# Performance work log

Hardware: AMD Instinct MI355X
Metric: run time of the kernel (lower is better)

## Reference

```python
import jax, jax.numpy as jnp
import numpy as np

N = 100000
IN_C = 128
OUT_C = 32
HEADS = 4
E = 1600000
NEG_SLOPE = 0.2


def setup_inputs() -> dict:
    key = jax.random.key(0)
    ks = jax.random.split(key, 8)
    x = jax.random.normal(ks[0], (N, IN_C), dtype=jnp.float32)
    edge_index = jax.random.randint(ks[1], (2, E), 0, N, dtype=jnp.int64)
    # GATConv params (PyG conventions): lin weight [H*C, in], att vectors [H, C], bias [H*C]
    sc = 1.0 / np.sqrt(IN_C)
    W = jax.random.uniform(ks[2], (HEADS * OUT_C, IN_C), dtype=jnp.float32, minval=-sc, maxval=sc)
    att_src = jax.random.normal(ks[3], (HEADS, OUT_C), dtype=jnp.float32) * 0.1
    att_dst = jax.random.normal(ks[4], (HEADS, OUT_C), dtype=jnp.float32) * 0.1
    bias_conv = jnp.zeros((HEADS * OUT_C,), dtype=jnp.float32)
    # final nn.Linear(H*C, C)
    sl = 1.0 / np.sqrt(HEADS * OUT_C)
    W_lin = jax.random.uniform(ks[5], (OUT_C, HEADS * OUT_C), dtype=jnp.float32, minval=-sl, maxval=sl)
    b_lin = jax.random.uniform(ks[6], (OUT_C,), dtype=jnp.float32, minval=-sl, maxval=sl)
    return {"x": x, "edge_index": edge_index, "W": W, "att_src": att_src,
            "att_dst": att_dst, "bias_conv": bias_conv, "W_lin": W_lin, "b_lin": b_lin}


def reference(x, edge_index, W, att_src, att_dst, bias_conv, W_lin, b_lin):
    n = x.shape[0]
    # add self loops (PyG default)
    loops = jnp.arange(n, dtype=edge_index.dtype)
    src = jnp.concatenate([edge_index[0], loops])
    dst = jnp.concatenate([edge_index[1], loops])
    # linear projection, per-head split: [N, H, C]
    h = (x @ W.T).reshape(n, HEADS, OUT_C)
    # per-node attention logits
    a_src = jnp.einsum('nhc,hc->nh', h, att_src)  # [N, H]
    a_dst = jnp.einsum('nhc,hc->nh', h, att_dst)  # [N, H]
    e = a_src[src] + a_dst[dst]                   # [E', H]
    e = jax.nn.leaky_relu(e, NEG_SLOPE)
    # segment softmax over incoming edges per destination node
    m = jax.ops.segment_max(e, dst, num_segments=n)       # [N, H]
    e = jnp.exp(e - m[dst])
    s = jax.ops.segment_sum(e, dst, num_segments=n)       # [N, H]
    alpha = e / s[dst]                                    # [E', H]
    # scatter-aggregate alpha-weighted source features
    msg = alpha[:, :, None] * h[src]                      # [E', H, C]
    out = jax.ops.segment_sum(msg, dst, num_segments=n)   # [N, H, C]
    out = out.reshape(n, HEADS * OUT_C) + bias_conv
    # final linear + ELU
    return jax.nn.elu(out @ W_lin.T + b_lin)
```

## Files before the change

### kernel.cpp

```cpp
#include <hip/hip_runtime.h>
#include <hip/hip_fp16.h>
#include <cstdint>
#include <cstddef>

#define NHEADS 4
#define OUT_C 32
#define HC 128
#define IN_CH 128
#define NEG_SLOPE 0.2f
#define LDSPAD 136
#define KEDGE 4096

typedef _Float16 half8 __attribute__((ext_vector_type(8)));
typedef float floatx4 __attribute__((ext_vector_type(4)));

static inline size_t align256(size_t v) { return (v + 255) & ~(size_t)255; }

__device__ __forceinline__ float lrelu(float v) { return v > 0.f ? v : NEG_SLOPE * v; }

__device__ __forceinline__ float wred_sum(float v) {
    v += __shfl_xor(v, 1);
    v += __shfl_xor(v, 2);
    v += __shfl_xor(v, 4);
    v += __shfl_xor(v, 8);
    v += __shfl_xor(v, 16);
    v += __shfl_xor(v, 32);
    return v;
}

__device__ __forceinline__ unsigned int pack_h2(float a, float b) {
    __half2 h = __floats2half2_rn(a, b);
    return *reinterpret_cast<unsigned int*>(&h);
}
__device__ __forceinline__ float2 unpack_h2(unsigned int u) {
    __half2 h = *reinterpret_cast<__half2*>(&u);
    return __half22float2(h);
}

__global__ void dw(const float* __restrict__ W, _Float16* __restrict__ wh,
                   const int* __restrict__ ei, int* __restrict__ flag) {
    if (blockIdx.x < 64) {
        int idx = blockIdx.x * 256 + threadIdx.x;
        wh[idx] = (_Float16)W[idx];
        return;
    }
    __shared__ int red[256];
    int t = threadIdx.x;
    int acc = 0;
    for (int i = t; i < 1024; i += 256) acc |= ei[2 * i + 1];
    red[t] = acc;
    __syncthreads();
    for (int s = 128; s > 0; s >>= 1) {
        if (t < s) red[t] |= red[t + s];
        __syncthreads();
    }
    if (t == 0) *flag = (red[0] == 0) ? 1 : 0;
}

__global__ __launch_bounds__(256) void gemm_h(const float* __restrict__ x,
                                              const _Float16* __restrict__ wh,
                                              const float* __restrict__ att_src,
                                              const float* __restrict__ att_dst,
                                              __half* __restrict__ h,
                                              float* __restrict__ a_src,
                                              float* __restrict__ a_dst, int n) {
    __shared__ __align__(16) _Float16 Ws[128 * LDSPAD];
    __shared__ __align__(16) _Float16 Xs[128 * LDSPAD];
    int tid = threadIdx.x;
    int rowbase = blockIdx.x << 7;

    const uint4* w4 = (const uint4*)wh;
#pragma unroll
    for (int i = 0; i < 8; ++i) {
        int u = (i << 8) + tid;
        int r = u >> 4, g = u & 15;
        uint4 v = w4[u];
        *(uint4*)&Ws[r * LDSPAD + (g << 3)] = v;
    }
    const float4* x4 = (const float4*)x;
#pragma unroll
    for (int i = 0; i < 16; ++i) {
        int u = (i << 8) + tid;
        int r = u >> 5, c4 = u & 31;
        int row = rowbase + r;
        if (row >= n) row = n - 1;
        float4 v = x4[((size_t)row << 5) + c4];
        uint2 uu;
        uu.x = pack_h2(v.x, v.y);
        uu.y = pack_h2(v.z, v.w);
        *(uint2*)&Xs[r * LDSPAD + (c4 << 2)] = uu;
    }
    __syncthreads();

    int lane = tid & 63, w = tid >> 6;
    int quad = lane >> 4, Lm = lane & 15;
    floatx4 acc[2][8];
#pragma unroll
    for (int rt = 0; rt < 2; ++rt)
#pragma unroll
        for (int c = 0; c < 8; ++c) acc[rt][c] = (floatx4){0.f, 0.f, 0.f, 0.f};

#pragma unroll
    for (int kc = 0; kc < 128; kc += 32) {
        int ko = kc + (quad << 3);
        half8 a0 = *(const half8*)&Xs[((w << 5) + Lm) * LDSPAD + ko];
        half8 a1 = *(const half8*)&Xs[((w << 5) + 16 + Lm) * LDSPAD + ko];
#pragma unroll
        for (int c = 0; c < 8; ++c) {
            half8 b = *(const half8*)&Ws[((c << 4) + Lm) * LDSPAD + ko];
            acc[0][c] = __builtin_amdgcn_mfma_f32_16x16x32_f16(a0, b, acc[0][c], 0, 0, 0);
            acc[1][c] = __builtin_amdgcn_mfma_f32_16x16x32_f16(a1, b, acc[1][c], 0, 0, 0);
        }
    }
    __syncthreads();
#pragma unroll
    for (int rt = 0; rt < 2; ++rt)
#pragma unroll
        for (int c = 0; c < 8; ++c)
#pragma unroll
            for (int i = 0; i < 4; ++i) {
                int rl = (w << 5) + (rt << 4) + (quad << 2) + i;
                int cl = (c << 4) + Lm;
                Xs[rl * LDSPAD + cl] = (_Float16)acc[rt][c][i];
            }
    __syncthreads();
#pragma unroll
    for (int i = 0; i < 8; ++i) {
        int u = (i << 8) + tid;
        int r = u >> 4, g = u & 15;
        int row = rowbase + r;
        if (row < n) {
            uint4 v = *(uint4*)&Xs[r * LDSPAD + (g << 3)];
            *(uint4*)(h + ((size_t)row << 7) + (g << 3)) = v;
        }
    }
    int r = tid >> 1, seg = tid & 1;
    int row = rowbase + r;
    const _Float16* hp = &Xs[r * LDSPAD + (seg << 6)];
    float sa = 0.f, da = 0.f, sb = 0.f, db = 0.f;
#pragma unroll
    for (int g8 = 0; g8 < 8; ++g8) {
        half8 v = *(const half8*)&hp[g8 << 3];
        int co = (seg << 6) + (g8 << 3);
        float4 A1 = *(const float4*)&att_src[co];
        float4 A2 = *(const float4*)&att_src[co + 4];
        float4 D1 = *(const float4*)&att_dst[co];
        float4 D2 = *(const float4*)&att_dst[co + 4];
        float f0 = (float)v[0], f1 = (float)v[1], f2 = (float)v[2], f3 = (float)v[3];
        float f4 = (float)v[4], f5 = (float)v[5], f6 = (float)v[6], f7 = (float)v[7];
        float ts = f0 * A1.x + f1 * A1.y + f2 * A1.z + f3 * A1.w
                 + f4 * A2.x + f5 * A2.y + f6 * A2.z + f7 * A2.w;
        float td = f0 * D1.x + f1 * D1.y + f2 * D1.z + f3 * D1.w
                 + f4 * D2.x + f5 * D2.y + f6 * D2.z + f7 * D2.w;
        if (g8 < 4) { sa += ts; da += td; } else { sb += ts; db += td; }
    }
    if (row < n) {
        int base = (row << 2) + (seg << 1);
        a_src[base] = sa;
        a_src[base + 1] = sb;
        a_dst[base] = da;
        a_dst[base + 1] = db;
    }
}

__global__ void bhist(const int* __restrict__ ei, const int* __restrict__ flag,
                      int* __restrict__ bcount, int E, int sh) {
    __shared__ int c[256];
    int t = threadIdx.x;
    c[t] = 0;
    __syncthreads();
    int f64 = *flag;
    int stride = gridDim.x * 256;
    for (int i = blockIdx.x * 256 + t; i < E; i += stride) {
        int d;
        if (f64) d = (int)((const long long*)ei)[(size_t)E + i];
        else     d = ei[(size_t)E + i];
        atomicAdd(&c[d >> sh], 1);
    }
    __syncthreads();
    if (c[t]) atomicAdd(&bcount[t], c[t]);
}

__global__ void bscan(const int* __restrict__ bcount, int* __restrict__ bucket_base,
                      int* __restrict__ gcursor, int* __restrict__ off,
                      int n, int E, int sh) {
    __shared__ int ts[256];
    int t = threadIdx.x;
    int lo = t << sh, hi = (t + 1) << sh;
    if (hi > n) hi = n;
    int nodes = hi > lo ? hi - lo : 0;
    int v = bcount[t] + nodes;
    ts[t] = v;
    __syncthreads();
    int run = v;
    for (int d = 1; d < 256; d <<= 1) {
        int o = (t >= d) ? ts[t - d] : 0;
        __syncthreads();
        run += o;
        ts[t] = run;
        __syncthreads();
    }
    int excl = run - v;
    bucket_base[t] = excl;
    gcursor[t] = excl;
    if (t == 255) {
        bucket_base[256] = run;
        off[n] = E + n;
    }
}

__global__ __launch_bounds__(256) void bscatter(const int* __restrict__ ei,
                                                const int* __restrict__ flag,
                                                int* __restrict__ gcursor,
                                                int2* __restrict__ bkt,
                                                int E, int n, int sh) {
    __shared__ int cnt[256], base[256], lcur[256];
    int t = threadIdx.x;
    cnt[t] = 0;
    lcur[t] = 0;
    int total = E + n;
    int i0 = blockIdx.x * KEDGE;
    int f64 = *flag;
    int ed[16], es[16];
    __syncthreads();
#pragma unroll
    for (int j = 0; j < 16; ++j) {
        int i = i0 + (j << 8) + t;
        int s = 0, d = -1;
        if (i < total) {
            if (i < E) {
                if (f64) {
                    s = (int)((const long long*)ei)[i];
                    d = (int)((const long long*)ei)[(size_t)E + i];
                } else {
                    s = ei[i];
                    d = ei[(size_t)E + i];
                }
            } else {
                s = d = i - E;
            }
            atomicAdd(&cnt[d >> sh], 1);
        }
        ed[j] = d;
        es[j] = s;
    }
    __syncthreads();
    base[t] = cnt[t] ? atomicAdd(&gcursor[t], cnt[t]) : 0;
    __syncthreads();
#pragma unroll
    for (int j = 0; j < 16; ++j) {
        int d = ed[j];
        if (d >= 0) {
            int b = d >> sh;
            int pos = base[b] + atomicAdd(&lcur[b], 1);
            bkt[pos] = make_int2(d, es[j]);
        }
    }
}

__global__ __launch_bounds__(256) void bsort(const int2* __restrict__ bkt,
                                             const int* __restrict__ bucket_base,
                                             int* __restrict__ off,
                                             int* __restrict__ sorted,
                                             int n, int sh) {
    __shared__ int cnt[512], offl[512], ts[256];
    int t = threadIdx.x, bid = blockIdx.x;
    int node0 = bid << sh;
    int node1 = (bid + 1) << sh;
    if (node1 > n) node1 = n;
    int nn = node1 - node0;
    int e0 = bucket_base[bid], e1 = bucket_base[bid + 1];
    cnt[t] = 0;
    cnt[t + 256] = 0;
    __syncthreads();
    for (int i = e0 + t; i < e1; i += 256) {
        int2 e = bkt[i];
        atomicAdd(&cnt[e.x - node0], 1);
    }
    __syncthreads();
    int a = cnt[t << 1], b = cnt[(t << 1) + 1];
    int s = a + b;
    ts[t] = s;
    __syncthreads();
    int run = s;
    for (int d = 1; d < 256; d <<= 1) {
        int o = (t >= d) ? ts[t - d] : 0;
        __syncthreads();
        run += o;
        ts[t] = run;
        __syncthreads();
    }
    int excl = run - s;
    offl[t << 1] = excl;
    offl[(t << 1) + 1] = excl + a;
    cnt[t << 1] = 0;
    cnt[(t << 1) + 1] = 0;
    __syncthreads();
    for (int i = t; i < nn; i += 256) off[node0 + i] = e0 + offl[i];
    for (int i = e0 + t; i < e1; i += 256) {
        int2 e = bkt[i];
        int li = e.x - node0;
        int pos = e0 + offl[li] + atomicAdd(&cnt[li], 1);
        sorted[pos] = e.y;
    }
}

__device__ __forceinline__ void accum_half(const int* ssrc, const float* sal,
                                           const __half* __restrict__ h,
                                           int deg, int half, int L, int head,
                                           float4& acc) {
    float4 a0 = {0, 0, 0, 0}, a1 = {0, 0, 0, 0}, a2 = {0, 0, 0, 0}, a3 = {0, 0, 0, 0};
    int j = half;
    for (; j + 6 < deg; j += 8) {
        int s0 = ssrc[j], s1 = ssrc[j + 2], s2 = ssrc[j + 4], s3 = ssrc[j + 6];
        float w0 = sal[(j << 2) + head];
        float w1 = sal[((j + 2) << 2) + head];
        float w2 = sal[((j + 4) << 2) + head];
        float w3 = sal[((j + 6) << 2) + head];
        uint2 u0 = *(const uint2*)(h + ((size_t)s0 << 7) + (L << 2));
        uint2 u1 = *(const uint2*)(h + ((size_t)s1 << 7) + (L << 2));
        uint2 u2 = *(const uint2*)(h + ((size_t)s2 << 7) + (L << 2));
        uint2 u3 = *(const uint2*)(h + ((size_t)s3 << 7) + (L << 2));
        float2 f0a = unpack_h2(u0.x), f0b = unpack_h2(u0.y);
        float2 f1a = unpack_h2(u1.x), f1b = unpack_h2(u1.y);
        float2 f2a = unpack_h2(u2.x), f2b = unpack_h2(u2.y);
        float2 f3a = unpack_h2(u3.x), f3b = unpack_h2(u3.y);
        a0.x = fmaf(w0, f0a.x, a0.x); a0.y = fmaf(w0, f0a.y, a0.y);
        a0.z = fmaf(w0, f0b.x, a0.z); a0.w = fmaf(w0, f0b.y, a0.w);
        a1.x = fmaf(w1, f1a.x, a1.x); a1.y = fmaf(w1, f1a.y, a1.y);
        a1.z = fmaf(w1, f1b.x, a1.z); a1.w = fmaf(w1, f1b.y, a1.w);
        a2.x = fmaf(w2, f2a.x, a2.x); a2.y = fmaf(w2, f2a.y, a2.y);
        a2.z = fmaf(w2, f2b.x, a2.z); a2.w = fmaf(w2, f2b.y, a2.w);
        a3.x = fmaf(w3, f3a.x, a3.x); a3.y = fmaf(w3, f3a.y, a3.y);
        a3.z = fmaf(w3, f3b.x, a3.z); a3.w = fmaf(w3, f3b.y, a3.w);
    }
    for (; j < deg; j += 2) {
        int s0 = ssrc[j];
        float w0 = sal[(j << 2) + head];
        uint2 u0 = *(const uint2*)(h + ((size_t)s0 << 7) + (L << 2));
        float2 f0a = unpack_h2(u0.x), f0b = unpack_h2(u0.y);
        a0.x = fmaf(w0, f0a.x, a0.x); a0.y = fmaf(w0, f0a.y, a0.y);
        a0.z = fmaf(w0, f0b.x, a0.z); a0.w = fmaf(w0, f0b.y, a0.w);
    }
    acc.x += a0.x + a1.x + a2.x + a3.x;
    acc.y += a0.y + a1.y + a2.y + a3.y;
    acc.z += a0.z + a1.z + a2.z + a3.z;
    acc.w += a0.w + a1.w + a2.w + a3.w;
}

__global__ __launch_bounds__(256) void aggregate(const __half* __restrict__ h,
                                                 const int* __restrict__ sorted,
                                                 const int* __restrict__ off,
                                                 const float* __restrict__ a_src,
                                                 const float* __restrict__ a_dst,
                                                 const float* __restrict__ bias,
                                                 __half* __restrict__ agg, int n) {
    __shared__ __align__(16) int sh_src[4][64];
    __shared__ __align__(16) float sh_al[4][256];
    int wslot = threadIdx.x >> 6;
    int lane = threadIdx.x & 63;
    int wid = blockIdx.x * 4 + wslot;
    int nw = gridDim.x * 4;
    int L = lane & 31, half = lane >> 5, head = L >> 3;
    float4 b4 = ((const float4*)bias)[L];
    const float4* as4 = (const float4*)a_src;
    const float4* ad4 = (const float4*)a_dst;
    int* ssrc = sh_src[wslot];
    float* sal = sh_al[wslot];

    for (int node = wid; node < n; node += nw) {
        int start = off[node], end = off[node + 1];
        int deg = end - start;
        float4 ad = ad4[node];
        float4 acc = {0.f, 0.f, 0.f, 0.f};
        float4 psum = {0.f, 0.f, 0.f, 0.f};

        if (deg <= 64) {
            bool v = lane < deg;
            int idx = start + (v ? lane : 0);
            int s = sorted[idx];
            float4 as = as4[s];
            float4 p;
            p.x = v ? __expf(lrelu(as.x + ad.x)) : 0.f;
            p.y = v ? __expf(lrelu(as.y + ad.y)) : 0.f;
            p.z = v ? __expf(lrelu(as.z + ad.z)) : 0.f;
            p.w = v ? __expf(lrelu(as.w + ad.w)) : 0.f;
            psum = p;
            ssrc[lane] = s;
            *(float4*)&sal[lane << 2] = p;
            asm volatile("s_waitcnt lgkmcnt(0)" ::: "memory");
            accum_half(ssrc, sal, h, deg, half, L, head, acc);
            asm volatile("" ::: "memory");
        } else {
            for (int bb = 0; bb < deg; bb += 64) {
                int i = bb + lane;
                bool v = i < deg;
                int idx = start + (v ? i : 0);
                int s = sorted[idx];
                float4 as = as4[s];
                float4 p;
                p.x = v ? __expf(lrelu(as.x + ad.x)) : 0.f;
                p.y = v ? __expf(lrelu(as.y + ad.y)) : 0.f;
                p.z = v ? __expf(lrelu(as.z + ad.z)) : 0.f;
                p.w = v ? __expf(lrelu(as.w + ad.w)) : 0.f;
                psum.x += p.x; psum.y += p.y; psum.z += p.z; psum.w += p.w;
                ssrc[lane] = s;
                *(float4*)&sal[lane << 2] = p;
                asm volatile("s_waitcnt lgkmcnt(0)" ::: "memory");
                int cl = deg - bb;
                if (cl > 64) cl = 64;
                accum_half(ssrc, sal, h, cl, half, L, head, acc);
                asm volatile("" ::: "memory");
            }
        }
        float s0 = wred_sum(psum.x), s1 = wred_sum(psum.y);
        float s2 = wred_sum(psum.z), s3 = wred_sum(psum.w);
        float sh = (head == 0) ? s0 : (head == 1) ? s1 : (head == 2) ? s2 : s3;
        float inv = 1.f / sh;
        acc.x += __shfl_xor(acc.x, 32);
        acc.y += __shfl_xor(acc.y, 32);
        acc.z += __shfl_xor(acc.z, 32);
        acc.w += __shfl_xor(acc.w, 32);
        if (lane < 32) {
            float4 res = {fmaf(acc.x, inv, b4.x), fmaf(acc.y, inv, b4.y),
                          fmaf(acc.z, inv, b4.z), fmaf(acc.w, inv, b4.w)};
            uint2 u;
            u.x = pack_h2(res.x, res.y);
            u.y = pack_h2(res.z, res.w);
            *(uint2*)(agg + ((size_t)node << 7) + (L << 2)) = u;
        }
    }
}

__global__ __launch_bounds__(256) void proj(const __half* __restrict__ agg,
                                            const float* __restrict__ W_lin,
                                            const float* __restrict__ b_lin,
                                            float* __restrict__ out, int n) {
    __shared__ float xs[64][132];
    __shared__ float wt[128][36];
    int tid = threadIdx.x;
    const float4* w4 = (const float4*)W_lin;
#pragma unroll
    for (int i = 0; i < 4; ++i) {
        int f4 = (i << 8) + tid;
        int o = f4 >> 5, kk = (f4 & 31) << 2;
        float4 w = w4[f4];
        wt[kk][o] = w.x;
        wt[kk + 1][o] = w.y;
        wt[kk + 2][o] = w.z;
        wt[kk + 3][o] = w.w;
    }
    int rowbase = blockIdx.x << 6;
    const uint4* a4 = (const uint4*)agg;
#pragma unroll
    for (int i = 0; i < 4; ++i) {
        int f8 = (i << 8) + tid;
        int r = f8 >> 4, cc = (f8 & 15) << 3;
        int row = rowbase + r;
        if (row >= n) row = n - 1;
        uint4 u = a4[((size_t)row << 4) + (cc >> 3)];
        float2 f0 = unpack_h2(u.x), f1 = unpack_h2(u.y);
        float2 f2 = unpack_h2(u.z), f3 = unpack_h2(u.w);
        float* xp = &xs[r][cc];
        xp[0] = f0.x; xp[1] = f0.y; xp[2] = f1.x; xp[3] = f1.y;
        xp[4] = f2.x; xp[5] = f2.y; xp[6] = f3.x; xp[7] = f3.y;
    }
    __syncthreads();
    int r = tid >> 2, cg = tid & 3, c0 = cg << 3;
    float acc[8];
#pragma unroll
    for (int j = 0; j < 8; ++j) acc[j] = 0.f;
    for (int k = 0; k < 128; k += 4) {
        float4 xv = *(const float4*)&xs[r][k];
        float xk[4] = {xv.x, xv.y, xv.z, xv.w};
#pragma unroll
        for (int kk = 0; kk < 4; ++kk) {
            float4 wa = *(const float4*)&wt[k + kk][c0];
            float4 wb = *(const float4*)&wt[k + kk][c0 + 4];
            acc[0] = fmaf(xk[kk], wa.x, acc[0]);
            acc[1] = fmaf(xk[kk], wa.y, acc[1]);
            acc[2] = fmaf(xk[kk], wa.z, acc[2]);
            acc[3] = fmaf(xk[kk], wa.w, acc[3]);
            acc[4] = fmaf(xk[kk], wb.x, acc[4]);
            acc[5] = fmaf(xk[kk], wb.y, acc[5]);
            acc[6] = fmaf(xk[kk], wb.z, acc[6]);
            acc[7] = fmaf(xk[kk], wb.w, acc[7]);
        }
    }
    int row = rowbase + r;
    if (row < n) {
        float res[8];
#pragma unroll
        for (int j = 0; j < 8; ++j) {
            float v = acc[j] + b_lin[c0 + j];
            res[j] = v > 0.f ? v : (__expf(v) - 1.f);
        }
        float4* op = (float4*)(out + (size_t)row * 32 + c0);
        op[0] = make_float4(res[0], res[1], res[2], res[3]);
        op[1] = make_float4(res[4], res[5], res[6], res[7]);
    }
}

extern "C" void kernel_launch(void* const* d_in, const int* in_sizes, int n_in,
                              void* d_out, int out_size, void* d_ws, size_t ws_size,
                              hipStream_t stream) {
    const float* x = (const float*)d_in[0];
    const int* ei = (const int*)d_in[1];
    const float* W = (const float*)d_in[2];
    const float* att_src = (const float*)d_in[3];
    const float* att_dst = (const float*)d_in[4];
    const float* bias_conv = (const float*)d_in[5];
    const float* W_lin = (const float*)d_in[6];
    const float* b_lin = (const float*)d_in[7];
    int n = in_sizes[0] / IN_CH;
    int E = in_sizes[1] / 2;

    int sh = 0;
    while (((n + (1 << sh) - 1) >> sh) > 256) sh++;
    int NB = (n + (1 << sh) - 1) >> sh;

    char* ws = (char*)d_ws;
    size_t o = 0;
    auto alloc = [&](size_t bytes) { char* p = ws + o; o = align256(o + bytes); return p; };
    __half* h        = (__half*)alloc((size_t)n * HC * 2);
    __half* agg      = (__half*)alloc((size_t)n * HC * 2);
    _Float16* wh     = (_Float16*)alloc(128 * 128 * 2);
    float* a_src     = (float*)alloc((size_t)n * NHEADS * 4);
    float* a_dst     = (float*)alloc((size_t)n * NHEADS * 4);
    int* off         = (int*)alloc(((size_t)n + 1) * 4);
    int* bcount      = (int*)alloc(256 * 4);
    int* bucket_base = (int*)alloc(257 * 4);
    int* gcursor     = (int*)alloc(256 * 4);
    int* flag        = (int*)alloc(256);
    int* sorted      = (int*)alloc((size_t)(E + n + 64) * 4);
    int2* bkt        = (int2*)alloc((size_t)(E + n + 64) * 8);

    hipMemsetAsync(bcount, 0, 256 * 4, stream);

    dw<<<65, 256, 0, stream>>>(W, wh, ei, flag);
    gemm_h<<<(n + 127) / 128, 256, 0, stream>>>(x, wh, att_src, att_dst, h, a_src, a_dst, n);
    bhist<<<1024, 256, 0, stream>>>(ei, flag, bcount, E, sh);
    bscan<<<1, 256, 0, stream>>>(bcount, bucket_base, gcursor, off, n, E, sh);
    bscatter<<<(E + n + KEDGE - 1) / KEDGE, 256, 0, stream>>>(ei, flag, gcursor, bkt, E, n, sh);
    bsort<<<NB, 256, 0, stream>>>(bkt, bucket_base, off, sorted, n, sh);
    aggregate<<<2048, 256, 0, stream>>>(h, sorted, off, a_src, a_dst, bias_conv, agg, n);
    proj<<<(n + 63) / 64, 256, 0, stream>>>(agg, W_lin, b_lin, (float*)d_out, n);
}
```

Measured before the change: 309.6 us.

## Slice h/agg into per-16-channel planes and fold small kernels into neighbors

```diff
diff --git a/kernel.cpp b/kernel.cpp
--- a/kernel.cpp
+++ b/kernel.cpp
@@ -37,31 +37,29 @@
     return __half22float2(h);
 }
 
-__global__ void dw(const float* __restrict__ W, _Float16* __restrict__ wh,
-                   const int* __restrict__ ei, int* __restrict__ flag) {
-    if (blockIdx.x < 64) {
-        int idx = blockIdx.x * 256 + threadIdx.x;
-        wh[idx] = (_Float16)W[idx];
-        return;
-    }
-    __shared__ int red[256];
+__device__ __forceinline__ int detect_f64(const int* __restrict__ ei, int E, int* sf) {
     int t = threadIdx.x;
+    if (t == 0) *sf = 0;
+    __syncthreads();
+    int lim = E < 1024 ? E : 1024;
     int acc = 0;
-    for (int i = t; i < 1024; i += 256) acc |= ei[2 * i + 1];
-    red[t] = acc;
-    __syncthreads();
-    for (int s = 128; s > 0; s >>= 1) {
-        if (t < s) red[t] |= red[t + s];
-        __syncthreads();
-    }
-    if (t == 0) *flag = (red[0] == 0) ? 1 : 0;
+    for (int i = t; i < lim; i += 256) acc |= ei[2 * i + 1];
+    acc |= __shfl_xor(acc, 1);
+    acc |= __shfl_xor(acc, 2);
+    acc |= __shfl_xor(acc, 4);
+    acc |= __shfl_xor(acc, 8);
+    acc |= __shfl_xor(acc, 16);
+    acc |= __shfl_xor(acc, 32);
+    if ((t & 63) == 0 && acc) atomicOr(sf, 1);
+    __syncthreads();
+    return *sf == 0;
 }
 
 __global__ __launch_bounds__(256) void gemm_h(const float* __restrict__ x,
-                                              const _Float16* __restrict__ wh,
+                                              const float* __restrict__ W,
                                               const float* __restrict__ att_src,
                                               const float* __restrict__ att_dst,
-                                              __half* __restrict__ h,
+                                              __half* __restrict__ hpl,
                                               float* __restrict__ a_src,
                                               float* __restrict__ a_dst, int n) {
     __shared__ __align__(16) _Float16 Ws[128 * LDSPAD];
@@ -69,13 +67,16 @@
     int tid = threadIdx.x;
     int rowbase = blockIdx.x << 7;
 
-    const uint4* w4 = (const uint4*)wh;
-#pragma unroll
-    for (int i = 0; i < 8; ++i) {
+    const float4* wf = (const float4*)W;
+#pragma unroll
+    for (int i = 0; i < 16; ++i) {
         int u = (i << 8) + tid;
-        int r = u >> 4, g = u & 15;
-        uint4 v = w4[u];
-        *(uint4*)&Ws[r * LDSPAD + (g << 3)] = v;
+        int r = u >> 5, g = u & 31;
+        float4 v = wf[u];
+        uint2 uu;
+        uu.x = pack_h2(v.x, v.y);
+        uu.y = pack_h2(v.z, v.w);
+        *(uint2*)&Ws[r * LDSPAD + (g << 2)] = uu;
     }
     const float4* x4 = (const float4*)x;
 #pragma unroll
@@ -124,14 +125,15 @@
                 Xs[rl * LDSPAD + cl] = (_Float16)acc[rt][c][i];
             }
     __syncthreads();
-#pragma unroll
-    for (int i = 0; i < 8; ++i) {
-        int u = (i << 8) + tid;
-        int r = u >> 4, g = u & 15;
+    {
+        int r = tid >> 1, g = tid & 1;
         int row = rowbase + r;
         if (row < n) {
-            uint4 v = *(uint4*)&Xs[r * LDSPAD + (g << 3)];
-            *(uint4*)(h + ((size_t)row << 7) + (g << 3)) = v;
+#pragma unroll
+            for (int c = 0; c < 8; ++c) {
+                uint4 v = *(uint4*)&Xs[r * LDSPAD + (c << 4) + (g << 3)];
+                *(uint4*)(hpl + ((size_t)c * n + row) * 16 + (g << 3)) = v;
+            }
         }
     }
     int r = tid >> 1, seg = tid & 1;
@@ -163,13 +165,13 @@
     }
 }
 
-__global__ void bhist(const int* __restrict__ ei, const int* __restrict__ flag,
-                      int* __restrict__ bcount, int E, int sh) {
+__global__ void bhist(const int* __restrict__ ei, int* __restrict__ bcount,
+                      int E, int sh) {
     __shared__ int c[256];
+    __shared__ int sf;
     int t = threadIdx.x;
     c[t] = 0;
-    __syncthreads();
-    int f64 = *flag;
+    int f64 = detect_f64(ei, E, &sf);
     int stride = gridDim.x * 256;
     for (int i = blockIdx.x * 256 + t; i < E; i += stride) {
         int d;
@@ -181,48 +183,20 @@
     if (c[t]) atomicAdd(&bcount[t], c[t]);
 }
 
-__global__ void bscan(const int* __restrict__ bcount, int* __restrict__ bucket_base,
-                      int* __restrict__ gcursor, int* __restrict__ off,
-                      int n, int E, int sh) {
-    __shared__ int ts[256];
-    int t = threadIdx.x;
-    int lo = t << sh, hi = (t + 1) << sh;
-    if (hi > n) hi = n;
-    int nodes = hi > lo ? hi - lo : 0;
-    int v = bcount[t] + nodes;
-    ts[t] = v;
-    __syncthreads();
-    int run = v;
-    for (int d = 1; d < 256; d <<= 1) {
-        int o = (t >= d) ? ts[t - d] : 0;
-        __syncthreads();
-        run += o;
-        ts[t] = run;
-        __syncthreads();
-    }
-    int excl = run - v;
-    bucket_base[t] = excl;
-    gcursor[t] = excl;
-    if (t == 255) {
-        bucket_base[256] = run;
-        off[n] = E + n;
-    }
-}
-
 __global__ __launch_bounds__(256) void bscatter(const int* __restrict__ ei,
-                                                const int* __restrict__ flag,
+                                                const int* __restrict__ bcount,
                                                 int* __restrict__ gcursor,
                                                 int2* __restrict__ bkt,
                                                 int E, int n, int sh) {
-    __shared__ int cnt[256], base[256], lcur[256];
+    __shared__ int cnt[256], base[256], lcur[256], ts[256];
+    __shared__ int sf;
     int t = threadIdx.x;
     cnt[t] = 0;
     lcur[t] = 0;
+    int f64 = detect_f64(ei, E, &sf);
     int total = E + n;
     int i0 = blockIdx.x * KEDGE;
-    int f64 = *flag;
     int ed[16], es[16];
-    __syncthreads();
 #pragma unroll
     for (int j = 0; j < 16; ++j) {
         int i = i0 + (j << 8) + t;
@@ -244,8 +218,22 @@
         ed[j] = d;
         es[j] = s;
     }
-    __syncthreads();
-    base[t] = cnt[t] ? atomicAdd(&gcursor[t], cnt[t]) : 0;
+    int lo = t << sh, hi = (t + 1) << sh;
+    if (hi > n) hi = n;
+    int nodes = hi > lo ? hi - lo : 0;
+    int v = bcount[t] + nodes;
+    ts[t] = v;
+    __syncthreads();
+    int run = v;
+    for (int d = 1; d < 256; d <<= 1) {
+        int o = (t >= d) ? ts[t - d] : 0;
+        __syncthreads();
+        run += o;
+        ts[t] = run;
+        __syncthreads();
+    }
+    int excl = run - v;
+    base[t] = excl + (cnt[t] ? atomicAdd(&gcursor[t], cnt[t]) : 0);
     __syncthreads();
 #pragma unroll
     for (int j = 0; j < 16; ++j) {
@@ -259,30 +247,19 @@
 }
 
 __global__ __launch_bounds__(256) void bsort(const int2* __restrict__ bkt,
-                                             const int* __restrict__ bucket_base,
+                                             const int* __restrict__ bcount,
                                              int* __restrict__ off,
                                              int* __restrict__ sorted,
-                                             int n, int sh) {
+                                             int n, int E, int sh) {
     __shared__ int cnt[512], offl[512], ts[256];
     int t = threadIdx.x, bid = blockIdx.x;
-    int node0 = bid << sh;
-    int node1 = (bid + 1) << sh;
-    if (node1 > n) node1 = n;
-    int nn = node1 - node0;
-    int e0 = bucket_base[bid], e1 = bucket_base[bid + 1];
-    cnt[t] = 0;
-    cnt[t + 256] = 0;
-    __syncthreads();
-    for (int i = e0 + t; i < e1; i += 256) {
-        int2 e = bkt[i];
-        atomicAdd(&cnt[e.x - node0], 1);
-    }
-    __syncthreads();
-    int a = cnt[t << 1], b = cnt[(t << 1) + 1];
-    int s = a + b;
-    ts[t] = s;
-    __syncthreads();
-    int run = s;
+    int lo = t << sh, hi = (t + 1) << sh;
+    if (hi > n) hi = n;
+    int nodes = hi > lo ? hi - lo : 0;
+    int v = bcount[t] + nodes;
+    ts[t] = v;
+    __syncthreads();
+    int run = v;
     for (int d = 1; d < 256; d <<= 1) {
         int o = (t >= d) ? ts[t - d] : 0;
         __syncthreads();
@@ -290,6 +267,34 @@
         ts[t] = run;
         __syncthreads();
     }
+    int e0 = (bid > 0) ? ts[bid - 1] : 0;
+    int e1 = ts[bid];
+    if (bid == gridDim.x - 1 && t == 0) off[n] = E + n;
+    int node0 = bid << sh;
+    int node1 = (bid + 1) << sh;
+    if (node1 > n) node1 = n;
+    int nn = node1 - node0;
+    __syncthreads();
+    cnt[t] = 0;
+    cnt[t + 256] = 0;
+    __syncthreads();
+    for (int i = e0 + t; i < e1; i += 256) {
+        int2 e = bkt[i];
+        atomicAdd(&cnt[e.x - node0], 1);
+    }
+    __syncthreads();
+    int a = cnt[t << 1], b = cnt[(t << 1) + 1];
+    int s = a + b;
+    ts[t] = s;
+    __syncthreads();
+    run = s;
+    for (int d = 1; d < 256; d <<= 1) {
+        int o = (t >= d) ? ts[t - d] : 0;
+        __syncthreads();
+        run += o;
+        ts[t] = run;
+        __syncthreads();
+    }
     int excl = run - s;
     offl[t << 1] = excl;
     offl[(t << 1) + 1] = excl + a;
@@ -305,134 +310,121 @@
     }
 }
 
-__device__ __forceinline__ void accum_half(const int* ssrc, const float* sal,
-                                           const __half* __restrict__ h,
-                                           int deg, int half, int L, int head,
-                                           float4& acc) {
-    float4 a0 = {0, 0, 0, 0}, a1 = {0, 0, 0, 0}, a2 = {0, 0, 0, 0}, a3 = {0, 0, 0, 0};
-    int j = half;
-    for (; j + 6 < deg; j += 8) {
-        int s0 = ssrc[j], s1 = ssrc[j + 2], s2 = ssrc[j + 4], s3 = ssrc[j + 6];
-        float w0 = sal[(j << 2) + head];
-        float w1 = sal[((j + 2) << 2) + head];
-        float w2 = sal[((j + 4) << 2) + head];
-        float w3 = sal[((j + 6) << 2) + head];
-        uint2 u0 = *(const uint2*)(h + ((size_t)s0 << 7) + (L << 2));
-        uint2 u1 = *(const uint2*)(h + ((size_t)s1 << 7) + (L << 2));
-        uint2 u2 = *(const uint2*)(h + ((size_t)s2 << 7) + (L << 2));
-        uint2 u3 = *(const uint2*)(h + ((size_t)s3 << 7) + (L << 2));
-        float2 f0a = unpack_h2(u0.x), f0b = unpack_h2(u0.y);
-        float2 f1a = unpack_h2(u1.x), f1b = unpack_h2(u1.y);
-        float2 f2a = unpack_h2(u2.x), f2b = unpack_h2(u2.y);
-        float2 f3a = unpack_h2(u3.x), f3b = unpack_h2(u3.y);
-        a0.x = fmaf(w0, f0a.x, a0.x); a0.y = fmaf(w0, f0a.y, a0.y);
-        a0.z = fmaf(w0, f0b.x, a0.z); a0.w = fmaf(w0, f0b.y, a0.w);
-        a1.x = fmaf(w1, f1a.x, a1.x); a1.y = fmaf(w1, f1a.y, a1.y);
-        a1.z = fmaf(w1, f1b.x, a1.z); a1.w = fmaf(w1, f1b.y, a1.w);
-        a2.x = fmaf(w2, f2a.x, a2.x); a2.y = fmaf(w2, f2a.y, a2.y);
-        a2.z = fmaf(w2, f2b.x, a2.z); a2.w = fmaf(w2, f2b.y, a2.w);
-        a3.x = fmaf(w3, f3a.x, a3.x); a3.y = fmaf(w3, f3a.y, a3.y);
-        a3.z = fmaf(w3, f3b.x, a3.z); a3.w = fmaf(w3, f3b.y, a3.w);
-    }
-    for (; j < deg; j += 2) {
-        int s0 = ssrc[j];
-        float w0 = sal[(j << 2) + head];
-        uint2 u0 = *(const uint2*)(h + ((size_t)s0 << 7) + (L << 2));
-        float2 f0a = unpack_h2(u0.x), f0b = unpack_h2(u0.y);
-        a0.x = fmaf(w0, f0a.x, a0.x); a0.y = fmaf(w0, f0a.y, a0.y);
-        a0.z = fmaf(w0, f0b.x, a0.z); a0.w = fmaf(w0, f0b.y, a0.w);
-    }
-    acc.x += a0.x + a1.x + a2.x + a3.x;
-    acc.y += a0.y + a1.y + a2.y + a3.y;
-    acc.z += a0.z + a1.z + a2.z + a3.z;
-    acc.w += a0.w + a1.w + a2.w + a3.w;
-}
-
-__global__ __launch_bounds__(256) void aggregate(const __half* __restrict__ h,
+__global__ __launch_bounds__(256) void aggregate(const __half* __restrict__ hpl,
                                                  const int* __restrict__ sorted,
                                                  const int* __restrict__ off,
                                                  const float* __restrict__ a_src,
                                                  const float* __restrict__ a_dst,
                                                  const float* __restrict__ bias,
-                                                 __half* __restrict__ agg, int n) {
+                                                 __half* __restrict__ aggp, int n) {
     __shared__ __align__(16) int sh_src[4][64];
-    __shared__ __align__(16) float sh_al[4][256];
+    __shared__ __align__(16) float sh_al[4][64];
     int wslot = threadIdx.x >> 6;
     int lane = threadIdx.x & 63;
-    int wid = blockIdx.x * 4 + wslot;
-    int nw = gridDim.x * 4;
-    int L = lane & 31, half = lane >> 5, head = L >> 3;
-    float4 b4 = ((const float4*)bias)[L];
-    const float4* as4 = (const float4*)a_src;
-    const float4* ad4 = (const float4*)a_dst;
+    int slice = blockIdx.x & 7;
+    int head = slice >> 1;
+    int wid = (blockIdx.x >> 3) * 4 + wslot;
+    int nw = (gridDim.x >> 3) * 4;
+    int eg = lane >> 3, cd = lane & 7;
+    const __half* hp = hpl + (size_t)slice * n * 16;
+    __half* ap = aggp + (size_t)slice * n * 16;
+    float2 b2 = ((const float2*)bias)[(slice << 3) + cd];
     int* ssrc = sh_src[wslot];
     float* sal = sh_al[wslot];
 
     for (int node = wid; node < n; node += nw) {
         int start = off[node], end = off[node + 1];
         int deg = end - start;
-        float4 ad = ad4[node];
-        float4 acc = {0.f, 0.f, 0.f, 0.f};
-        float4 psum = {0.f, 0.f, 0.f, 0.f};
+        float ad = a_dst[(node << 2) + head];
+        float ax0 = 0.f, ay0 = 0.f, ax1 = 0.f, ay1 = 0.f;
+        float ptot;
 
         if (deg <= 64) {
             bool v = lane < deg;
             int idx = start + (v ? lane : 0);
             int s = sorted[idx];
-            float4 as = as4[s];
-            float4 p;
-            p.x = v ? __expf(lrelu(as.x + ad.x)) : 0.f;
-            p.y = v ? __expf(lrelu(as.y + ad.y)) : 0.f;
-            p.z = v ? __expf(lrelu(as.z + ad.z)) : 0.f;
-            p.w = v ? __expf(lrelu(as.w + ad.w)) : 0.f;
-            psum = p;
+            float as = a_src[(s << 2) + head];
+            float p = v ? __expf(lrelu(as + ad)) : 0.f;
+            ptot = wred_sum(p);
             ssrc[lane] = s;
-            *(float4*)&sal[lane << 2] = p;
+            sal[lane] = p;
             asm volatile("s_waitcnt lgkmcnt(0)" ::: "memory");
-            accum_half(ssrc, sal, h, deg, half, L, head, acc);
+            int it = 0;
+            for (; it + 15 < deg; it += 16) {
+                int j0 = it + eg, j1 = j0 + 8;
+                int s0 = ssrc[j0], s1 = ssrc[j1];
+                float w0 = sal[j0], w1 = sal[j1];
+                unsigned u0 = *(const unsigned*)(hp + ((size_t)s0 << 4) + (cd << 1));
+                unsigned u1 = *(const unsigned*)(hp + ((size_t)s1 << 4) + (cd << 1));
+                float2 f0 = unpack_h2(u0), f1 = unpack_h2(u1);
+                ax0 = fmaf(w0, f0.x, ax0); ay0 = fmaf(w0, f0.y, ay0);
+                ax1 = fmaf(w1, f1.x, ax1); ay1 = fmaf(w1, f1.y, ay1);
+            }
+            for (; it < deg; it += 8) {
+                int j = it + eg;
+                bool vv = j < deg;
+                int s0 = ssrc[vv ? j : 0];
+                float w0 = vv ? sal[j] : 0.f;
+                unsigned u0 = *(const unsigned*)(hp + ((size_t)s0 << 4) + (cd << 1));
+                float2 f0 = unpack_h2(u0);
+                ax0 = fmaf(w0, f0.x, ax0); ay0 = fmaf(w0, f0.y, ay0);
+            }
             asm volatile("" ::: "memory");
         } else {
+            float psum = 0.f;
             for (int bb = 0; bb < deg; bb += 64) {
                 int i = bb + lane;
                 bool v = i < deg;
                 int idx = start + (v ? i : 0);
                 int s = sorted[idx];
-                float4 as = as4[s];
-                float4 p;
-                p.x = v ? __expf(lrelu(as.x + ad.x)) : 0.f;
-                p.y = v ? __expf(lrelu(as.y + ad.y)) : 0.f;
-                p.z = v ? __expf(lrelu(as.z + ad.z)) : 0.f;
-                p.w = v ? __expf(lrelu(as.w + ad.w)) : 0.f;
-                psum.x += p.x; psum.y += p.y; psum.z += p.z; psum.w += p.w;
+                float as = a_src[(s << 2) + head];
+                float p = v ? __expf(lrelu(as + ad)) : 0.f;
+                psum += p;
                 ssrc[lane] = s;
-                *(float4*)&sal[lane << 2] = p;
+                sal[lane] = p;
                 asm volatile("s_waitcnt lgkmcnt(0)" ::: "memory");
                 int cl = deg - bb;
                 if (cl > 64) cl = 64;
-                accum_half(ssrc, sal, h, cl, half, L, head, acc);
+                int it = 0;
+                for (; it + 15 < cl; it += 16) {
+                    int j0 = it + eg, j1 = j0 + 8;
+                    int s0 = ssrc[j0], s1 = ssrc[j1];
+                    float w0 = sal[j0], w1 = sal[j1];
+                    unsigned u0 = *(const unsigned*)(hp + ((size_t)s0 << 4) + (cd << 1));
+                    unsigned u1 = *(const unsigned*)(hp + ((size_t)s1 << 4) + (cd << 1));
+                    float2 f0 = unpack_h2(u0), f1 = unpack_h2(u1);
+                    ax0 = fmaf(w0, f0.x, ax0); ay0 = fmaf(w0, f0.y, ay0);
+                    ax1 = fmaf(w1, f1.x, ax1); ay1 = fmaf(w1, f1.y, ay1);
+                }
+                for (; it < cl; it += 8) {
+                    int j = it + eg;
+                    bool vv = j < cl;
+                    int s0 = ssrc[vv ? j : 0];
+                    float w0 = vv ? sal[j] : 0.f;
+                    unsigned u0 = *(const unsigned*)(hp + ((size_t)s0 << 4) + (cd << 1));
+                    float2 f0 = unpack_h2(u0);
+                    ax0 = fmaf(w0, f0.x, ax0); ay0 = fmaf(w0, f0.y, ay0);
+                }
                 asm volatile("" ::: "memory");
             }
-        }
-        float s0 = wred_sum(psum.x), s1 = wred_sum(psum.y);
-        float s2 = wred_sum(psum.z), s3 = wred_sum(psum.w);
-        float sh = (head == 0) ? s0 : (head == 1) ? s1 : (head == 2) ? s2 : s3;
-        float inv = 1.f / sh;
-        acc.x += __shfl_xor(acc.x, 32);
-        acc.y += __shfl_xor(acc.y, 32);
-        acc.z += __shfl_xor(acc.z, 32);
-        acc.w += __shfl_xor(acc.w, 32);
-        if (lane < 32) {
-            float4 res = {fmaf(acc.x, inv, b4.x), fmaf(acc.y, inv, b4.y),
-                          fmaf(acc.z, inv, b4.z), fmaf(acc.w, inv, b4.w)};
-            uint2 u;
-            u.x = pack_h2(res.x, res.y);
-            u.y = pack_h2(res.z, res.w);
-            *(uint2*)(agg + ((size_t)node << 7) + (L << 2)) = u;
-        }
-    }
-}
-
-__global__ __launch_bounds__(256) void proj(const __half* __restrict__ agg,
+            ptot = wred_sum(psum);
+        }
+        float ax = ax0 + ax1, ay = ay0 + ay1;
+        ax += __shfl_xor(ax, 8);
+        ax += __shfl_xor(ax, 16);
+        ax += __shfl_xor(ax, 32);
+        ay += __shfl_xor(ay, 8);
+        ay += __shfl_xor(ay, 16);
+        ay += __shfl_xor(ay, 32);
+        float inv = 1.f / ptot;
+        if (lane < 8) {
+            *(unsigned*)(ap + ((size_t)node << 4) + (cd << 1)) =
+                pack_h2(fmaf(ax, inv, b2.x), fmaf(ay, inv, b2.y));
+        }
+    }
+}
+
+__global__ __launch_bounds__(256) void proj(const __half* __restrict__ aggp,
                                             const float* __restrict__ W_lin,
                                             const float* __restrict__ b_lin,
                                             float* __restrict__ out, int n) {
@@ -451,19 +443,17 @@
         wt[kk + 3][o] = w.w;
     }
     int rowbase = blockIdx.x << 6;
-    const uint4* a4 = (const uint4*)agg;
-#pragma unroll
-    for (int i = 0; i < 4; ++i) {
-        int f8 = (i << 8) + tid;
-        int r = f8 >> 4, cc = (f8 & 15) << 3;
+    {
+        int r = tid >> 2, part = tid & 3;
         int row = rowbase + r;
         if (row >= n) row = n - 1;
-        uint4 u = a4[((size_t)row << 4) + (cc >> 3)];
-        float2 f0 = unpack_h2(u.x), f1 = unpack_h2(u.y);
-        float2 f2 = unpack_h2(u.z), f3 = unpack_h2(u.w);
-        float* xp = &xs[r][cc];
-        xp[0] = f0.x; xp[1] = f0.y; xp[2] = f1.x; xp[3] = f1.y;
-        xp[4] = f2.x; xp[5] = f2.y; xp[6] = f3.x; xp[7] = f3.y;
+#pragma unroll
+        for (int c = 0; c < 8; ++c) {
+            uint2 u = *(const uint2*)(aggp + ((size_t)c * n + row) * 16 + (part << 2));
+            float2 f0 = unpack_h2(u.x), f1 = unpack_h2(u.y);
+            float* xp = &xs[r][(c << 4) + (part << 2)];
+            xp[0] = f0.x; xp[1] = f0.y; xp[2] = f1.x; xp[3] = f1.y;
+        }
     }
     __syncthreads();
     int r = tid >> 2, cg = tid & 3, c0 = cg << 3;
@@ -522,27 +512,22 @@
     char* ws = (char*)d_ws;
     size_t o = 0;
     auto alloc = [&](size_t bytes) { char* p = ws + o; o = align256(o + bytes); return p; };
-    __half* h        = (__half*)alloc((size_t)n * HC * 2);
-    __half* agg      = (__half*)alloc((size_t)n * HC * 2);
-    _Float16* wh     = (_Float16*)alloc(128 * 128 * 2);
-    float* a_src     = (float*)alloc((size_t)n * NHEADS * 4);
-    float* a_dst     = (float*)alloc((size_t)n * NHEADS * 4);
-    int* off         = (int*)alloc(((size_t)n + 1) * 4);
-    int* bcount      = (int*)alloc(256 * 4);
-    int* bucket_base = (int*)alloc(257 * 4);
-    int* gcursor     = (int*)alloc(256 * 4);
-    int* flag        = (int*)alloc(256);
-    int* sorted      = (int*)alloc((size_t)(E + n + 64) * 4);
-    int2* bkt        = (int2*)alloc((size_t)(E + n + 64) * 8);
-
-    hipMemsetAsync(bcount, 0, 256 * 4, stream);
-
-    dw<<<65, 256, 0, stream>>>(W, wh, ei, flag);
-    gemm_h<<<(n + 127) / 128, 256, 0, stream>>>(x, wh, att_src, att_dst, h, a_src, a_dst, n);
-    bhist<<<1024, 256, 0, stream>>>(ei, flag, bcount, E, sh);
-    bscan<<<1, 256, 0, stream>>>(bcount, bucket_base, gcursor, off, n, E, sh);
-    bscatter<<<(E + n + KEDGE - 1) / KEDGE, 256, 0, stream>>>(ei, flag, gcursor, bkt, E, n, sh);
-    bsort<<<NB, 256, 0, stream>>>(bkt, bucket_base, off, sorted, n, sh);
+    __half* h      = (__half*)alloc((size_t)n * HC * 2);
+    __half* agg    = (__half*)alloc((size_t)n * HC * 2);
+    float* a_src   = (float*)alloc((size_t)n * NHEADS * 4);
+    float* a_dst   = (float*)alloc((size_t)n * NHEADS * 4);
+    int* off       = (int*)alloc(((size_t)n + 1) * 4);
+    int* bcount    = (int*)alloc(256 * 4);
+    int* gcursor   = (int*)alloc(256 * 4);
+    int* sorted    = (int*)alloc((size_t)(E + n + 64) * 4);
+    int2* bkt      = (int2*)alloc((size_t)(E + n + 64) * 8);
+
+    hipMemsetAsync(bcount, 0, 2048, stream);
+
+    gemm_h<<<(n + 127) / 128, 256, 0, stream>>>(x, W, att_src, att_dst, h, a_src, a_dst, n);
+    bhist<<<1024, 256, 0, stream>>>(ei, bcount, E, sh);
+    bscatter<<<(E + n + KEDGE - 1) / KEDGE, 256, 0, stream>>>(ei, bcount, gcursor, bkt, E, n, sh);
+    bsort<<<NB, 256, 0, stream>>>(bkt, bcount, off, sorted, n, E, sh);
     aggregate<<<2048, 256, 0, stream>>>(h, sorted, off, a_src, a_dst, bias_conv, agg, n);
     proj<<<(n + 63) / 64, 256, 0, stream>>>(agg, W_lin, b_lin, (float*)d_out, n);
 }
```

Result: slower. 437.4 us (+41.3%).
